# Optimization experiments

Hardware: AMD Instinct MI355X
Metric: run time of the kernel (lower is better)

Reference implementation:

```python
import jax, jax.numpy as jnp
import numpy as np

NUM_NODES = 10000
NUM_EDGES = 640000
INPUT_DIM = 128
HIDDEN_DIM = 128


def setup_inputs() -> dict:
    key = jax.random.key(0)
    k_x, k_e, k_w1, k_b1, k_w2, k_b2 = jax.random.split(key, 6)
    x = jax.random.normal(k_x, (NUM_NODES, INPUT_DIM), dtype=jnp.float32)
    edge_index = jax.random.randint(k_e, (NUM_EDGES, 2), 0, NUM_NODES, dtype=jnp.int64)
    # MLP params (torch Linear: y = x @ W.T + b; store W already transposed as [in, out])
    s1 = 1.0 / np.sqrt(INPUT_DIM)
    s2 = 1.0 / np.sqrt(HIDDEN_DIM)
    W1 = jax.random.uniform(k_w1, (INPUT_DIM, HIDDEN_DIM), jnp.float32, -s1, s1)
    b1 = jax.random.uniform(k_b1, (HIDDEN_DIM,), jnp.float32, -s1, s1)
    W2 = jax.random.uniform(k_w2, (HIDDEN_DIM, HIDDEN_DIM), jnp.float32, -s2, s2)
    b2 = jax.random.uniform(k_b2, (HIDDEN_DIM,), jnp.float32, -s2, s2)
    return {"x": x, "edge_index": edge_index, "W1": W1, "b1": b1, "W2": W2, "b2": b2}


def reference(x, edge_index, W1, b1, W2, b2):
    # GIN aggregation: sum of neighbor features along edges (row <- col) + self loop.
    row = edge_index[:, 0]
    col = edge_index[:, 1]
    # scatter-add gathered neighbor features into destination nodes
    agg = jax.ops.segment_sum(x[col], row, num_segments=NUM_NODES)
    agg = agg + x  # self-loop contribution (identity edges appended in torch code)
    # 2-layer MLP: Linear -> ReLU -> Linear
    h = jnp.maximum(agg @ W1 + b1, 0.0)
    return h @ W2 + b2
```

## Files before the change

kernel.cpp:

```cpp
#include <hip/hip_runtime.h>

#define NN   10000
#define NE   640000
#define DIM  128
#define NTILES (NN / 16)
#define NBIN  320
#define NCHUNK 313
#define CAPC  32
#define EPB   2048
#define WPACK_BLOCKS 128
#define CONV_THREADS 160000
#define CONV_BLOCKS 625
#define BUILD_BLOCKS (NCHUNK + WPACK_BLOCKS + CONV_BLOCKS)
#define CLCAP 512

typedef __attribute__((ext_vector_type(8))) short bf16x8;
typedef __attribute__((ext_vector_type(8))) unsigned short u16x8;
typedef __attribute__((ext_vector_type(4))) float f32x4;

__device__ inline unsigned short f2bf(float f) {
    unsigned u = __builtin_bit_cast(unsigned, f);
    unsigned r = (u + 0x7fffu + ((u >> 16) & 1u)) >> 16;
    return (unsigned short)r;
}
__device__ inline float bf2f(unsigned short u) {
    return __builtin_bit_cast(float, (unsigned)u << 16);
}

#define OFF_CHUNK 400640
#define OFF_XB    13221120
#define OFF_W1P   15781120
#define OFF_W2P   15813888
#define WS_NEED   15846656

__global__ __launch_bounds__(256) void build_kernel(
        const int* __restrict__ ei, const float* __restrict__ x,
        const float* __restrict__ W1, const float* __restrict__ W2,
        int* __restrict__ cnt, unsigned* __restrict__ chunkmem,
        unsigned short* __restrict__ xb,
        unsigned short* __restrict__ W1p, unsigned short* __restrict__ W2p) {
    const int t = threadIdx.x;
    if (blockIdx.x < NCHUNK) {
        __shared__ int hist[NBIN];
        for (int b = t; b < NBIN; b += 256) hist[b] = 0;
        __syncthreads();
        const int e0 = blockIdx.x * EPB;
        #pragma unroll
        for (int i = 0; i < 8; ++i) {
            int idx = e0 + i * 256 + t;
            if (idx < NE) {
                int2 rc = *reinterpret_cast<const int2*>(ei + 2 * idx);
                int bn = rc.x >> 5;
                unsigned pk = ((unsigned)(rc.x & 31) << 14) | (unsigned)rc.y;
                int rk = atomicAdd(&hist[bn], 1);
                if (rk < CAPC)
                    chunkmem[((size_t)bn * NCHUNK + blockIdx.x) * CAPC + rk] = pk;
            }
        }
        __syncthreads();
        for (int b = t; b < NBIN; b += 256)
            cnt[blockIdx.x * NBIN + b] = hist[b];
    } else if (blockIdx.x < NCHUNK + WPACK_BLOCKS) {
        int id = (blockIdx.x - NCHUNK) * 256 + t;
        const float* W = (id < 16384) ? W1 : W2;
        unsigned short* Wp = (id < 16384) ? W1p : W2p;
        int f = id & 16383;
        int e = f & 7, lane = (f >> 3) & 63, kt = (f >> 9) & 3, nt = f >> 11;
        int kglob = kt * 32 + (lane >> 4) * 8 + e;
        int jglob = nt * 16 + (lane & 15);
        Wp[f] = f2bf(W[kglob * DIM + jglob]);
    } else {
        int pid = (blockIdx.x - NCHUNK - WPACK_BLOCKS) * 256 + t;
        if (pid < CONV_THREADS) {
            int i = pid * 8;
            float4 a = *reinterpret_cast<const float4*>(x + i);
            float4 b = *reinterpret_cast<const float4*>(x + i + 4);
            u16x8 pk;
            pk[0] = f2bf(a.x); pk[1] = f2bf(a.y); pk[2] = f2bf(a.z); pk[3] = f2bf(a.w);
            pk[4] = f2bf(b.x); pk[5] = f2bf(b.y); pk[6] = f2bf(b.z); pk[7] = f2bf(b.w);
            *reinterpret_cast<u16x8*>(xb + i) = pk;
        }
    }
}

__global__ __launch_bounds__(256) void gather_mlp_kernel(
        const unsigned short* __restrict__ xb,
        const int* __restrict__ cnt,
        const unsigned* __restrict__ chunkmem,
        const unsigned short* __restrict__ W1p,
        const unsigned short* __restrict__ W2p,
        const float* __restrict__ b1,
        const float* __restrict__ b2,
        float* __restrict__ out) {
    __shared__ __align__(16) unsigned short aggs[16][136];
    __shared__ __align__(16) unsigned short hbuf[16][136];
    __shared__ __align__(16) unsigned short clist[16][CLCAP];
    __shared__ int lcnt[16];

    const int row0 = blockIdx.x * 16;
    const int t = threadIdx.x;

    if (t < 16) lcnt[t] = 0;
    __syncthreads();
    {
        const int bin  = blockIdx.x >> 1;
        const int half = blockIdx.x & 1;
        for (int c = t; c < NCHUNK; c += 256) {
            int cn = cnt[c * NBIN + bin];
            cn = (cn > CAPC) ? CAPC : cn;
            const unsigned* ch = chunkmem + ((size_t)bin * NCHUNK + c) * CAPC;
            for (int k = 0; k < cn; ++k) {
                unsigned p = ch[k];
                int rl = p >> 14;
                if ((rl >> 4) == half) {
                    int n = rl & 15;
                    int slot = atomicAdd(&lcnt[n], 1);
                    if (slot < CLCAP)
                        clist[n][slot] = (unsigned short)(p & 0x3FFFu);
                }
            }
        }
    }
    __syncthreads();

    {
        const int n = t >> 4, l = t & 15;
        int deg = lcnt[n];
        deg = (deg > CLCAP) ? CLCAP : deg;
        const size_t lo = l * 8;

        float a0[8], a1[8], a2[8], a3[8];
        {
            u16x8 v = *reinterpret_cast<const u16x8*>(xb + (size_t)(row0 + n) * DIM + lo);
            #pragma unroll
            for (int j = 0; j < 8; ++j) { a0[j] = bf2f(v[j]); a1[j] = 0.f; a2[j] = 0.f; a3[j] = 0.f; }
        }
        int k = 0;
        for (; k + 4 <= deg; k += 4) {
            int c0 = clist[n][k + 0];
            int c1 = clist[n][k + 1];
            int c2 = clist[n][k + 2];
            int c3 = clist[n][k + 3];
            u16x8 v0 = *reinterpret_cast<const u16x8*>(xb + (size_t)c0 * DIM + lo);
            u16x8 v1 = *reinterpret_cast<const u16x8*>(xb + (size_t)c1 * DIM + lo);
            u16x8 v2 = *reinterpret_cast<const u16x8*>(xb + (size_t)c2 * DIM + lo);
            u16x8 v3 = *reinterpret_cast<const u16x8*>(xb + (size_t)c3 * DIM + lo);
            #pragma unroll
            for (int j = 0; j < 8; ++j) {
                a0[j] += bf2f(v0[j]);
                a1[j] += bf2f(v1[j]);
                a2[j] += bf2f(v2[j]);
                a3[j] += bf2f(v3[j]);
            }
        }
        for (; k < deg; ++k) {
            int c = clist[n][k];
            u16x8 v = *reinterpret_cast<const u16x8*>(xb + (size_t)c * DIM + lo);
            #pragma unroll
            for (int j = 0; j < 8; ++j) a0[j] += bf2f(v[j]);
        }
        u16x8 pk;
        #pragma unroll
        for (int j = 0; j < 8; ++j) pk[j] = f2bf((a0[j] + a1[j]) + (a2[j] + a3[j]));
        *reinterpret_cast<u16x8*>(&aggs[n][l * 8]) = pk;
    }
    __syncthreads();

    const int wid  = t >> 6;
    const int lane = t & 63;
    const int r16  = lane & 15;
    const int kg   = lane >> 4;
    const int drow = kg * 4;

    bf16x8 af[4];
    #pragma unroll
    for (int kt = 0; kt < 4; ++kt)
        af[kt] = *reinterpret_cast<const bf16x8*>(&aggs[r16][kt * 32 + kg * 8]);

    const f32x4 zero = {0.f, 0.f, 0.f, 0.f};
    f32x4 acc1[2] = {zero, zero};
    #pragma unroll
    for (int kt = 0; kt < 4; ++kt) {
        #pragma unroll
        for (int q = 0; q < 2; ++q) {
            int nt = wid * 2 + q;
            bf16x8 w = *reinterpret_cast<const bf16x8*>(
                W1p + ((nt * 4 + kt) * 64 + lane) * 8);
            acc1[q] = __builtin_amdgcn_mfma_f32_16x16x32_bf16(af[kt], w, acc1[q], 0, 0, 0);
        }
    }
    #pragma unroll
    for (int q = 0; q < 2; ++q) {
        int nt = wid * 2 + q;
        float bv = b1[nt * 16 + r16];
        #pragma unroll
        for (int r = 0; r < 4; ++r) {
            float h = fmaxf(acc1[q][r] + bv, 0.0f);
            hbuf[drow + r][nt * 16 + r16] = f2bf(h);
        }
    }
    __syncthreads();

    bf16x8 hf[4];
    #pragma unroll
    for (int kt = 0; kt < 4; ++kt)
        hf[kt] = *reinterpret_cast<const bf16x8*>(&hbuf[r16][kt * 32 + kg * 8]);

    f32x4 acc2[2] = {zero, zero};
    #pragma unroll
    for (int kt = 0; kt < 4; ++kt) {
        #pragma unroll
        for (int q = 0; q < 2; ++q) {
            int nt = wid * 2 + q;
            bf16x8 w = *reinterpret_cast<const bf16x8*>(
                W2p + ((nt * 4 + kt) * 64 + lane) * 8);
            acc2[q] = __builtin_amdgcn_mfma_f32_16x16x32_bf16(hf[kt], w, acc2[q], 0, 0, 0);
        }
    }
    #pragma unroll
    for (int q = 0; q < 2; ++q) {
        int nt = wid * 2 + q;
        float bv = b2[nt * 16 + r16];
        #pragma unroll
        for (int r = 0; r < 4; ++r)
            out[(size_t)(row0 + drow + r) * DIM + nt * 16 + r16] = acc2[q][r] + bv;
    }
}

__global__ void fb_zero_kernel(int* __restrict__ p, int n) {
    int i = blockIdx.x * blockDim.x + threadIdx.x;
    if (i < n) p[i] = 0;
}
__global__ void fb_count_kernel(const int* __restrict__ ei, int* __restrict__ deg) {
    int e = blockIdx.x * blockDim.x + threadIdx.x;
    if (e < NE) atomicAdd(&deg[ei[2 * e]], 1);
}
__global__ __launch_bounds__(1024) void fb_scan_kernel(const int* __restrict__ deg,
                                                       int* __restrict__ rowptr) {
    __shared__ int wtot[16];
    const int t = threadIdx.x;
    const int base = t * 10;
    int local[10];
    int s = 0;
    #pragma unroll
    for (int i = 0; i < 10; ++i) {
        int v = (base + i < NN) ? deg[base + i] : 0;
        local[i] = s;
        s += v;
    }
    const int mySum = s;
    #pragma unroll
    for (int off = 1; off < 64; off <<= 1) {
        int v = __shfl_up(s, (unsigned)off, 64);
        if ((t & 63) >= off) s += v;
    }
    if ((t & 63) == 63) wtot[t >> 6] = s;
    __syncthreads();
    if (t == 0) {
        int run = 0;
        #pragma unroll
        for (int i = 0; i < 16; ++i) { int v = wtot[i]; wtot[i] = run; run += v; }
    }
    __syncthreads();
    const int ex = wtot[t >> 6] + (s - mySum);
    #pragma unroll
    for (int i = 0; i < 10; ++i)
        if (base + i < NN) rowptr[base + i] = ex + local[i];
    if (t == 1023) rowptr[NN] = ex + mySum;
}
__global__ void fb_fill_kernel(const int* __restrict__ ei, const int* __restrict__ rowptr,
                               int* __restrict__ fill, int* __restrict__ colidx) {
    int e = blockIdx.x * blockDim.x + threadIdx.x;
    if (e < NE) {
        int r = ei[2 * e], c = ei[2 * e + 1];
        colidx[rowptr[r] + atomicAdd(&fill[r], 1)] = c;
    }
}
__global__ __launch_bounds__(128) void fb_gather_kernel(const float* __restrict__ x,
                                                        const int* __restrict__ rowptr,
                                                        const int* __restrict__ colidx,
                                                        float* __restrict__ agg) {
    const int n = blockIdx.x, j = threadIdx.x;
    const int s = rowptr[n], e = rowptr[n + 1];
    float acc = x[(size_t)n * DIM + j];
    float a0 = 0.f, a1 = 0.f, a2 = 0.f, a3 = 0.f;
    int k = s;
    for (; k + 4 <= e; k += 4) {
        a0 += x[(size_t)colidx[k + 0] * DIM + j];
        a1 += x[(size_t)colidx[k + 1] * DIM + j];
        a2 += x[(size_t)colidx[k + 2] * DIM + j];
        a3 += x[(size_t)colidx[k + 3] * DIM + j];
    }
    for (; k < e; ++k) acc += x[(size_t)colidx[k] * DIM + j];
    agg[(size_t)n * DIM + j] = acc + (a0 + a1) + (a2 + a3);
}
__global__ __launch_bounds__(512) void fb_mlp_kernel(
        const float* __restrict__ agg,
        const float* __restrict__ W1, const float* __restrict__ b1,
        const float* __restrict__ W2, const float* __restrict__ b2,
        float* __restrict__ out) {
    __shared__ float w1s[DIM * DIM];
    __shared__ float w2s[DIM * DIM];
    __shared__ float b1s[DIM], b2s[DIM];
    __shared__ float as[4][DIM], hs[4][DIM];
    for (int i = threadIdx.x; i < DIM * DIM; i += blockDim.x) { w1s[i] = W1[i]; w2s[i] = W2[i]; }
    if (threadIdx.x < DIM) { b1s[threadIdx.x] = b1[threadIdx.x]; b2s[threadIdx.x] = b2[threadIdx.x]; }
    __syncthreads();
    const int r = threadIdx.x >> 7, j = threadIdx.x & 127;
    for (int base = blockIdx.x * 4; base < NN; base += gridDim.x * 4) {
        int rowid = base + r;
        as[r][j] = (rowid < NN) ? agg[(size_t)rowid * DIM + j] : 0.0f;
        __syncthreads();
        float acc = b1s[j];
        #pragma unroll 8
        for (int k = 0; k < DIM; ++k) acc = fmaf(as[r][k], w1s[k * DIM + j], acc);
        hs[r][j] = fmaxf(acc, 0.0f);
        __syncthreads();
        float acc2 = b2s[j];
        #pragma unroll 8
        for (int k = 0; k < DIM; ++k) acc2 = fmaf(hs[r][k], w2s[k * DIM + j], acc2);
        if (rowid < NN) out[(size_t)rowid * DIM + j] = acc2;
        __syncthreads();
    }
}

extern "C" void kernel_launch(void* const* d_in, const int* in_sizes, int n_in,
                              void* d_out, int out_size, void* d_ws, size_t ws_size,
                              hipStream_t stream) {
    const float* x  = (const float*)d_in[0];
    const int*   ei = (const int*)d_in[1];
    const float* W1 = (const float*)d_in[2];
    const float* b1 = (const float*)d_in[3];
    const float* W2 = (const float*)d_in[4];
    const float* b2 = (const float*)d_in[5];
    float* out = (float*)d_out;

    if (ws_size >= WS_NEED) {
        char* ws = (char*)d_ws;
        int* cnt = (int*)ws;
        unsigned* chunkmem = (unsigned*)(ws + OFF_CHUNK);
        unsigned short* xb  = (unsigned short*)(ws + OFF_XB);
        unsigned short* W1p = (unsigned short*)(ws + OFF_W1P);
        unsigned short* W2p = (unsigned short*)(ws + OFF_W2P);

        build_kernel<<<BUILD_BLOCKS, 256, 0, stream>>>(
            ei, x, W1, W2, cnt, chunkmem, xb, W1p, W2p);
        gather_mlp_kernel<<<NTILES, 256, 0, stream>>>(
            xb, cnt, chunkmem, W1p, W2p, b1, b2, out);
    } else {
        int* wsI    = (int*)d_ws;
        int* deg    = wsI;
        int* fillc  = wsI + 10240;
        int* rowptr = wsI + 20480;
        int* colidx = wsI + 30720;
        const size_t csr_bytes = (size_t)(30720 + NE) * sizeof(int);
        const size_t agg_bytes = (size_t)NN * DIM * sizeof(float);
        float* agg = (ws_size >= csr_bytes + agg_bytes)
                         ? (float*)((char*)d_ws + csr_bytes) : out;

        fb_zero_kernel<<<(20480 + 255) / 256, 256, 0, stream>>>(deg, 20480);
        fb_count_kernel<<<(NE + 255) / 256, 256, 0, stream>>>(ei, deg);
        fb_scan_kernel<<<1, 1024, 0, stream>>>(deg, rowptr);
        fb_fill_kernel<<<(NE + 255) / 256, 256, 0, stream>>>(ei, rowptr, fillc, colidx);
        fb_gather_kernel<<<NN, 128, 0, stream>>>(x, rowptr, colidx, agg);
        fb_mlp_kernel<<<256, 512, 0, stream>>>(agg, W1, b1, W2, b2, out);
    }
}
```

Before: 38.68 us.

## Double gather block to 512 threads, splitting neighbor lists across halves

The fused gather+MLP kernel now runs 512 threads per block. Each node's neighbor list is split into two halves summed by separate thread groups, and the partials are combined through a new fp32 shared buffer. The MLP stage is reassigned to eight waves, each computing one 16-column tile instead of two. The goal is more memory-level parallelism for the latency-bound irregular gathers, at the cost of extra shared memory, another barrier and possibly lower occupancy.

```diff
diff --git a/kernel.cpp b/kernel.cpp
--- a/kernel.cpp
+++ b/kernel.cpp
@@ -83,7 +83,7 @@
     }
 }
 
-__global__ __launch_bounds__(256) void gather_mlp_kernel(
+__global__ __launch_bounds__(512) void gather_mlp_kernel(
         const unsigned short* __restrict__ xb,
         const int* __restrict__ cnt,
         const unsigned* __restrict__ chunkmem,
@@ -95,6 +95,7 @@
     __shared__ __align__(16) unsigned short aggs[16][136];
     __shared__ __align__(16) unsigned short hbuf[16][136];
     __shared__ __align__(16) unsigned short clist[16][CLCAP];
+    __shared__ __align__(16) float paggs[16][128];
     __shared__ int lcnt[16];
 
     const int row0 = blockIdx.x * 16;
@@ -105,7 +106,7 @@
     {
         const int bin  = blockIdx.x >> 1;
         const int half = blockIdx.x & 1;
-        for (int c = t; c < NCHUNK; c += 256) {
+        for (int c = t; c < NCHUNK; c += 512) {
             int cn = cnt[c * NBIN + bin];
             cn = (cn > CAPC) ? CAPC : cn;
             const unsigned* ch = chunkmem + ((size_t)bin * NCHUNK + c) * CAPC;
@@ -124,19 +125,26 @@
     __syncthreads();
 
     {
-        const int n = t >> 4, l = t & 15;
+        const int h = t >> 8;
+        const int n = (t >> 4) & 15;
+        const int l = t & 15;
         int deg = lcnt[n];
         deg = (deg > CLCAP) ? CLCAP : deg;
+        const int mid = (deg + 1) >> 1;
+        const int k0 = h ? mid : 0;
+        const int k1 = h ? deg : mid;
         const size_t lo = l * 8;
 
         float a0[8], a1[8], a2[8], a3[8];
-        {
+        #pragma unroll
+        for (int j = 0; j < 8; ++j) { a0[j] = 0.f; a1[j] = 0.f; a2[j] = 0.f; a3[j] = 0.f; }
+        if (h == 0) {
             u16x8 v = *reinterpret_cast<const u16x8*>(xb + (size_t)(row0 + n) * DIM + lo);
             #pragma unroll
-            for (int j = 0; j < 8; ++j) { a0[j] = bf2f(v[j]); a1[j] = 0.f; a2[j] = 0.f; a3[j] = 0.f; }
-        }
-        int k = 0;
-        for (; k + 4 <= deg; k += 4) {
+            for (int j = 0; j < 8; ++j) a0[j] = bf2f(v[j]);
+        }
+        int k = k0;
+        for (; k + 4 <= k1; k += 4) {
             int c0 = clist[n][k + 0];
             int c1 = clist[n][k + 1];
             int c2 = clist[n][k + 2];
@@ -153,16 +161,27 @@
                 a3[j] += bf2f(v3[j]);
             }
         }
-        for (; k < deg; ++k) {
+        for (; k < k1; ++k) {
             int c = clist[n][k];
             u16x8 v = *reinterpret_cast<const u16x8*>(xb + (size_t)c * DIM + lo);
             #pragma unroll
             for (int j = 0; j < 8; ++j) a0[j] += bf2f(v[j]);
         }
-        u16x8 pk;
-        #pragma unroll
-        for (int j = 0; j < 8; ++j) pk[j] = f2bf((a0[j] + a1[j]) + (a2[j] + a3[j]));
-        *reinterpret_cast<u16x8*>(&aggs[n][l * 8]) = pk;
+        float s[8];
+        #pragma unroll
+        for (int j = 0; j < 8; ++j) s[j] = (a0[j] + a1[j]) + (a2[j] + a3[j]);
+
+        if (h == 1) {
+            #pragma unroll
+            for (int j = 0; j < 8; ++j) paggs[n][l * 8 + j] = s[j];
+        }
+        __syncthreads();
+        if (h == 0) {
+            u16x8 pk;
+            #pragma unroll
+            for (int j = 0; j < 8; ++j) pk[j] = f2bf(s[j] + paggs[n][l * 8 + j]);
+            *reinterpret_cast<u16x8*>(&aggs[n][l * 8]) = pk;
+        }
     }
     __syncthreads();
 
@@ -178,25 +197,19 @@
         af[kt] = *reinterpret_cast<const bf16x8*>(&aggs[r16][kt * 32 + kg * 8]);
 
     const f32x4 zero = {0.f, 0.f, 0.f, 0.f};
-    f32x4 acc1[2] = {zero, zero};
+    f32x4 acc1 = zero;
     #pragma unroll
     for (int kt = 0; kt < 4; ++kt) {
-        #pragma unroll
-        for (int q = 0; q < 2; ++q) {
-            int nt = wid * 2 + q;
-            bf16x8 w = *reinterpret_cast<const bf16x8*>(
-                W1p + ((nt * 4 + kt) * 64 + lane) * 8);
-            acc1[q] = __builtin_amdgcn_mfma_f32_16x16x32_bf16(af[kt], w, acc1[q], 0, 0, 0);
-        }
-    }
-    #pragma unroll
-    for (int q = 0; q < 2; ++q) {
-        int nt = wid * 2 + q;
-        float bv = b1[nt * 16 + r16];
+        bf16x8 w = *reinterpret_cast<const bf16x8*>(
+            W1p + ((wid * 4 + kt) * 64 + lane) * 8);
+        acc1 = __builtin_amdgcn_mfma_f32_16x16x32_bf16(af[kt], w, acc1, 0, 0, 0);
+    }
+    {
+        float bv = b1[wid * 16 + r16];
         #pragma unroll
         for (int r = 0; r < 4; ++r) {
-            float h = fmaxf(acc1[q][r] + bv, 0.0f);
-            hbuf[drow + r][nt * 16 + r16] = f2bf(h);
+            float h = fmaxf(acc1[r] + bv, 0.0f);
+            hbuf[drow + r][wid * 16 + r16] = f2bf(h);
         }
     }
     __syncthreads();
@@ -206,24 +219,18 @@
     for (int kt = 0; kt < 4; ++kt)
         hf[kt] = *reinterpret_cast<const bf16x8*>(&hbuf[r16][kt * 32 + kg * 8]);
 
-    f32x4 acc2[2] = {zero, zero};
+    f32x4 acc2 = zero;
     #pragma unroll
     for (int kt = 0; kt < 4; ++kt) {
-        #pragma unroll
-        for (int q = 0; q < 2; ++q) {
-            int nt = wid * 2 + q;
-            bf16x8 w = *reinterpret_cast<const bf16x8*>(
-                W2p + ((nt * 4 + kt) * 64 + lane) * 8);
-            acc2[q] = __builtin_amdgcn_mfma_f32_16x16x32_bf16(hf[kt], w, acc2[q], 0, 0, 0);
-        }
-    }
-    #pragma unroll
-    for (int q = 0; q < 2; ++q) {
-        int nt = wid * 2 + q;
-        float bv = b2[nt * 16 + r16];
+        bf16x8 w = *reinterpret_cast<const bf16x8*>(
+            W2p + ((wid * 4 + kt) * 64 + lane) * 8);
+        acc2 = __builtin_amdgcn_mfma_f32_16x16x32_bf16(hf[kt], w, acc2, 0, 0, 0);
+    }
+    {
+        float bv = b2[wid * 16 + r16];
         #pragma unroll
         for (int r = 0; r < 4; ++r)
-            out[(size_t)(row0 + drow + r) * DIM + nt * 16 + r16] = acc2[q][r] + bv;
+            out[(size_t)(row0 + drow + r) * DIM + wid * 16 + r16] = acc2[r] + bv;
     }
 }
 
@@ -345,7 +352,7 @@
 
         build_kernel<<<BUILD_BLOCKS, 256, 0, stream>>>(
             ei, x, W1, W2, cnt, chunkmem, xb, W1p, W2p);
-        gather_mlp_kernel<<<NTILES, 256, 0, stream>>>(
+        gather_mlp_kernel<<<NTILES, 512, 0, stream>>>(
             xb, cnt, chunkmem, W1p, W2p, b1, b2, out);
     } else {
         int* wsI    = (int*)d_ws;
```

Result: faster. 36.01 us (median of 2 runs) (-6.9%).
